# Optimization experiments

Hardware: AMD Instinct MI355X
Metric: run time of the kernel (lower is better)

The kernel has to match this reference:

```python
import jax, jax.numpy as jnp
import numpy as np

N_ATOMS = 100000
N_EDGES = 6400000
CUTOFF = 12.0
CUTOFF_SR = 2.0
CUTOFF_SQ = CUTOFF * CUTOFF
KEHALF = 7.199822675975274  # ASE kehalf, unit factors = 1


def poly6_switch(d, cutoff):
    # Poly6 smooth switch-off: 1 at d=0, 0 at d>=cutoff
    x = d / cutoff
    sw = 1.0 - 10.0 * x**3 + 15.0 * x**4 - 6.0 * x**5
    return jnp.where(d < cutoff, sw, jnp.zeros_like(sw))


def setup_inputs() -> dict:
    key = jax.random.key(0)
    k1, k2, k3, k4, k5 = jax.random.split(key, 5)
    atomic_charges = jax.random.normal(k1, (N_ATOMS,), dtype=jnp.float32) * 0.3
    atomic_dipoles = jax.random.normal(k2, (N_ATOMS,), dtype=jnp.float32) * 0.1
    # distances in (0.5, 13.5): some pairs inside short-range, some beyond cutoff
    distances = jax.random.uniform(k3, (N_EDGES,), dtype=jnp.float32) * 13.0 + 0.5
    idx_i = jax.random.randint(k4, (N_EDGES,), 0, N_ATOMS, dtype=jnp.int32)
    idx_j = jax.random.randint(k5, (N_EDGES,), 0, N_ATOMS, dtype=jnp.int32)
    return {
        "atomic_charges": atomic_charges,
        "atomic_dipoles": atomic_dipoles,
        "distances": distances,
        "idx_i": idx_i,
        "idx_j": idx_j,
    }


def reference(atomic_charges, atomic_dipoles, distances, idx_i, idx_j):
    # gather per-edge charges / dipoles
    qi = atomic_charges[idx_i]
    qj = atomic_charges[idx_j]
    di = atomic_dipoles[idx_i]
    dj = atomic_dipoles[idx_j]

    d = distances
    d_sh = jnp.sqrt(d * d + 1.0)  # shielded distance

    sw_off = poly6_switch(d, CUTOFF_SR)
    sw_on = 1.0 - sw_off

    # split_distance=True branch (cutoff != cutoff_short_range):
    # shifted-force Coulomb (charge-charge, ~1/d)
    E_ord_q = 1.0 / d + d / CUTOFF_SQ - 2.0 / CUTOFF
    E_sh_q = 1.0 / d_sh + d_sh / CUTOFF_SQ - 2.0 / CUTOFF
    E_q = KEHALF * qi * qj * (sw_off * E_sh_q + sw_on * E_ord_q)

    # dipole-dipole term (~1/d^3), same shielded/ordinary blending
    E_ord_d = 1.0 / d**3
    E_sh_d = 1.0 / d_sh**3
    E_d = KEHALF * di * dj * (sw_off * E_sh_d + sw_on * E_ord_d)

    E = E_q + E_d
    E = jnp.where(d <= CUTOFF, E, jnp.zeros_like(E))

    # scatter-sum per-edge energies to atoms
    return jax.ops.segment_sum(E, idx_i, num_segments=N_ATOMS)
```

## Files before the change

kernel.cpp:

```cpp
#include <hip/hip_runtime.h>
#include <hip/hip_bf16.h>
#include <hip/hip_fp16.h>

#define CUTOFF_C    12.0f
#define CUTOFF_SR_C 2.0f
#define CUTOFF_SQ_C 144.0f
#define KEHALF_C    7.199822675975274f

#define BLK1   1024

#define CH_DUO   17408
#define LUT_DUO  1024
#define CH_SOLO  33792
#define LUT_SOLO 2048

__device__ __forceinline__ float edge_energy(float d, float qi, float qj,
                                             float di, float dj) {
    float inv_d   = __frcp_rn(d);
    float dsh     = __fsqrt_rn(fmaf(d, d, 1.0f));
    float inv_dsh = __frcp_rn(dsh);
    float x  = d * (1.0f / CUTOFF_SR_C);
    float x3 = x * x * x;
    float sw = fmaf(x3, fmaf(x, fmaf(x, -6.0f, 15.0f), -10.0f), 1.0f);
    float sw_off = (d < CUTOFF_SR_C) ? sw : 0.0f;
    float Eoq = inv_d   + fmaf(d,   (1.0f / CUTOFF_SQ_C), -(2.0f / CUTOFF_C));
    float Esq = inv_dsh + fmaf(dsh, (1.0f / CUTOFF_SQ_C), -(2.0f / CUTOFF_C));
    float Eq  = (KEHALF_C * qi * qj) * fmaf(sw_off, Esq - Eoq, Eoq);
    float Eod = inv_d * inv_d * inv_d;
    float Esd = inv_dsh * inv_dsh * inv_dsh;
    float Ed  = (KEHALF_C * di * dj) * fmaf(sw_off, Esd - Eod, Eod);
    return Eq + Ed;
}

__device__ __forceinline__ float2 fg_exact(float d) {
    float inv_d   = 1.0f / d;
    float dsh     = sqrtf(fmaf(d, d, 1.0f));
    float inv_dsh = 1.0f / dsh;
    float x  = d * (1.0f / CUTOFF_SR_C);
    float x3 = x * x * x;
    float sw = fmaf(x3, fmaf(x, fmaf(x, -6.0f, 15.0f), -10.0f), 1.0f);
    float sw_off = (d < CUTOFF_SR_C) ? sw : 0.0f;
    float Foq = inv_d   + fmaf(d,   (1.0f / CUTOFF_SQ_C), -(2.0f / CUTOFF_C));
    float Fsq = inv_dsh + fmaf(dsh, (1.0f / CUTOFF_SQ_C), -(2.0f / CUTOFF_C));
    float F   = fmaf(sw_off, Fsq - Foq, Foq);
    float God = inv_d * inv_d * inv_d;
    float Gsd = inv_dsh * inv_dsh * inv_dsh;
    float G   = fmaf(sw_off, Gsd - God, God);
    return make_float2(KEHALF_C * F, KEHALF_C * G);
}

__device__ __forceinline__ __half2 vw_make_exact(float d, __half2 hqdj) {
    float2 qdj = __half22float2(hqdj);
    float2 fg  = fg_exact(d);
    return __floats2half2_rn(qdj.x * fg.x, qdj.y * fg.y);
}

__device__ __forceinline__ unsigned h2bits(__half2 h) {
    union { __half2 h; unsigned u; } c; c.h = h; return c.u;
}
__device__ __forceinline__ __half2 bits2h(unsigned u) {
    union { unsigned u; __half2 h; } c; c.u = u; return c.h;
}
template <typename T>
__device__ __forceinline__ auto atom_add_h2(T* p, T v, int)
    -> decltype(atomicAdd(p, v), void()) {
    atomicAdd(p, v);
}
template <typename T>
__device__ __forceinline__ void atom_add_h2(T* p, T v, long) {
    unsigned* u = (unsigned*)p;
    unsigned old = *u, assumed;
    do {
        assumed = old;
        __half2 sum = __hadd2(bits2h(assumed), v);
        old = atomicCAS(u, assumed, h2bits(sum));
    } while (old != assumed);
}

__global__ __launch_bounds__(256) void pc_pack_qd_h(
    const float* __restrict__ q,
    const float* __restrict__ dip,
    __half2*     __restrict__ qd,
    int n_atoms)
{
    int a = blockIdx.x * 256 + threadIdx.x;
    if (a < n_atoms) qd[a] = __floats2half2_rn(q[a], dip[a]);
}

template <int CH, int LUTN, int BLK>
__global__ __launch_bounds__(BLK) void pc_scatter_lut(
    const float*   __restrict__ dist,
    const int*     __restrict__ idx_i,
    const int*     __restrict__ idx_j,
    const __half2* __restrict__ qd,
    __half2*       __restrict__ partial,
    int n_edges, int n4, int S, int gps, int n_atoms, int nch)
{
    extern __shared__ char smem[];
    __half2* acc2 = (__half2*)smem;
    float2*  lut  = (float2*)(smem + (size_t)CH * sizeof(__half2));

    const int s    = blockIdx.x % S;
    const int c    = blockIdx.x / S;
    const int base = c * CH;
    const int lim  = min(CH, n_atoms - base);

    const __half2 hzero = __floats2half2_rn(0.0f, 0.0f);
    for (int i = threadIdx.x; i < CH; i += BLK) acc2[i] = hzero;

    const float hstep = CUTOFF_C / (float)LUTN;
    for (int k = threadIdx.x; k <= LUTN; k += BLK) {
        float d = fmaxf((float)k * hstep, 0.25f * hstep);
        lut[k] = fg_exact(d);
    }
    __syncthreads();

    const int g0 = s * gps;
    const int g1 = min(g0 + gps, n4);
    const int4*   idxi4 = (const int4*)idx_i;
    const int4*   idxj4 = (const int4*)idx_j;
    const float4* dist4 = (const float4*)dist;
    const float   dscale = (float)LUTN / CUTOFF_C;

    for (int g = g0 + (int)threadIdx.x; g < g1; g += BLK) {
        int4   i4 = idxi4[g];
        int4   j4 = idxj4[g];
        float4 d4 = dist4[g];

        int      ii[4] = { i4.x, i4.y, i4.z, i4.w };
        int      jj[4] = { j4.x, j4.y, j4.z, j4.w };
        float    dd[4] = { d4.x, d4.y, d4.z, d4.w };
        unsigned lc[4];
        bool     vl[4];
        __half2  qh[4];

        #pragma unroll
        for (int k = 0; k < 4; ++k) {
            lc[k] = (unsigned)(ii[k] - base);
            vl[k] = (lc[k] < (unsigned)CH) && (dd[k] <= CUTOFF_C);
        }
        #pragma unroll
        for (int k = 0; k < 4; ++k)
            qh[k] = vl[k] ? qd[jj[k]] : hzero;

        #pragma unroll
        for (int k = 0; k < 4; ++k) {
            if (vl[k]) {
                float t  = dd[k] * dscale;
                int   kk = min((int)t, LUTN - 1);
                float fr = t - (float)kk;
                float2 l0 = lut[kk];
                float2 l1 = lut[kk + 1];
                float F = fmaf(fr, l1.x - l0.x, l0.x);
                float G = fmaf(fr, l1.y - l0.y, l0.y);
                float2 qdj = __half22float2(qh[k]);
                __half2 vw = __floats2half2_rn(qdj.x * F, qdj.y * G);
                atom_add_h2(&acc2[lc[k]], vw, 0);
            }
        }
    }

    if (s == S - 1) {
        for (int e = (n4 << 2) + (int)threadIdx.x; e < n_edges; e += BLK) {
            int i = idx_i[e];
            float d = dist[e];
            unsigned local = (unsigned)(i - base);
            if (local < (unsigned)CH && d <= CUTOFF_C) {
                __half2 vw = vw_make_exact(d, qd[idx_j[e]]);
                atom_add_h2(&acc2[local], vw, 0);
            }
        }
    }

    __syncthreads();
    __half2* row = partial + (size_t)s * n_atoms + base;
    for (int i = threadIdx.x; i < lim; i += BLK) row[i] = acc2[i];
}

__global__ __launch_bounds__(256) void pc_reduce_vw(
    const __half2* __restrict__ partial,
    const float*   __restrict__ q,
    const float*   __restrict__ dip,
    float*         __restrict__ out,
    int n_atoms, int S)
{
    __shared__ float2 sh[256];
    int a0   = blockIdx.x * 64;
    int lane = threadIdx.x & 63;
    int w    = threadIdx.x >> 6;
    int a    = a0 + lane;

    float sv = 0.0f, sw = 0.0f;
    if (a < n_atoms) {
        int per = S >> 2;
        const __half2* p = partial + a;
        int s = w * per, send = s + per;
        for (; s < send; ++s) {
            float2 t = __half22float2(p[(size_t)s * n_atoms]);
            sv += t.x; sw += t.y;
        }
    }
    sh[threadIdx.x] = make_float2(sv, sw);
    __syncthreads();
    if (w == 0 && a < n_atoms) {
        float2 t0 = sh[lane],       t1 = sh[64 + lane];
        float2 t2 = sh[128 + lane], t3 = sh[192 + lane];
        float fv = (t0.x + t1.x) + (t2.x + t3.x);
        float fw = (t0.y + t1.y) + (t2.y + t3.y);
        out[a] = fmaf(q[a], fv, dip[a] * fw);
    }
}

__global__ __launch_bounds__(256) void pc_dipole_edges_atomic(
    const float* __restrict__ q,
    const float* __restrict__ dip,
    const float* __restrict__ dist,
    const int*   __restrict__ idx_i,
    const int*   __restrict__ idx_j,
    float*       __restrict__ out,
    int n_edges)
{
    int t = blockIdx.x * blockDim.x + threadIdx.x;
    const int stride = gridDim.x * blockDim.x;
    for (int e = t; e < n_edges; e += stride) {
        float d = dist[e];
        if (d > CUTOFF_C) continue;
        int i = idx_i[e], j = idx_j[e];
        atomicAdd(&out[i], edge_energy(d, q[i], q[j], dip[i], dip[j]));
    }
}

static int probe_blocks(const void* f, int blk, size_t lds) {
    hipError_t e1 = hipFuncSetAttribute(
        f, hipFuncAttributeMaxDynamicSharedMemorySize, (int)lds);
    int nb = 0;
    hipError_t e2 = hipOccupancyMaxActiveBlocksPerMultiprocessor(&nb, f, blk, lds);
    if (e1 != hipSuccess || e2 != hipSuccess) return 0;
    return nb;
}

extern "C" void kernel_launch(void* const* d_in, const int* in_sizes, int n_in,
                              void* d_out, int out_size, void* d_ws, size_t ws_size,
                              hipStream_t stream) {
    const float* q     = (const float*)d_in[0];
    const float* dip   = (const float*)d_in[1];
    const float* dist  = (const float*)d_in[2];
    const int*   idx_i = (const int*)d_in[3];
    const int*   idx_j = (const int*)d_in[4];
    float*       out   = (float*)d_out;

    int n_edges = in_sizes[2];
    int n_atoms = out_size;
    int n4      = n_edges >> 2;

    size_t lds_duo  = (size_t)CH_DUO  * sizeof(__half2)
                    + (size_t)(LUT_DUO  + 1) * sizeof(float2);
    size_t lds_solo = (size_t)CH_SOLO * sizeof(__half2)
                    + (size_t)(LUT_SOLO + 1) * sizeof(float2);

    int nb_duo = probe_blocks((const void*)&pc_scatter_lut<CH_DUO, LUT_DUO, BLK1>,
                              BLK1, lds_duo);
    int nb_solo = probe_blocks((const void*)&pc_scatter_lut<CH_SOLO, LUT_SOLO, BLK1>,
                               BLK1, lds_solo);

    bool use_duo = (nb_duo >= 2);
    int  CH, nch, S, cap;
    size_t lds;
    if (use_duo) {
        CH  = CH_DUO;  lds = lds_duo;
        nch = (n_atoms + CH - 1) / CH;
        cap = 512;
    } else {
        CH  = CH_SOLO; lds = lds_solo;
        nch = (n_atoms + CH - 1) / CH;
        cap = 256;
    }
    S = (cap / nch) & ~7;
    if (S < 8) S = 8;

    size_t qd_b  = ((size_t)n_atoms * sizeof(__half2) + 255) & ~(size_t)255;
    size_t avail = (ws_size > qd_b) ? ws_size - qd_b : 0;
    int S_fit = (int)(avail / ((size_t)n_atoms * sizeof(__half2)));
    if (S_fit < S) S = S_fit & ~7;

    bool ok = (use_duo || nb_solo >= 1) && S >= 8 && n_atoms > 0;

    if (ok) {
        __half2* qd      = (__half2*)d_ws;
        __half2* partial = (__half2*)((char*)d_ws + qd_b);
        int      gps     = (n4 + S - 1) / S;

        pc_pack_qd_h<<<(n_atoms + 255) / 256, 256, 0, stream>>>(q, dip, qd,
                                                                n_atoms);
        if (use_duo)
            pc_scatter_lut<CH_DUO, LUT_DUO, BLK1>
                <<<S * nch, BLK1, lds, stream>>>(
                    dist, idx_i, idx_j, qd, partial, n_edges, n4, S, gps,
                    n_atoms, nch);
        else
            pc_scatter_lut<CH_SOLO, LUT_SOLO, BLK1>
                <<<S * nch, BLK1, lds, stream>>>(
                    dist, idx_i, idx_j, qd, partial, n_edges, n4, S, gps,
                    n_atoms, nch);
        pc_reduce_vw<<<(n_atoms + 63) / 64, 256, 0, stream>>>(
            partial, q, dip, out, n_atoms, S);
    } else {
        hipMemsetAsync(out, 0, (size_t)n_atoms * sizeof(float), stream);
        int grid = (n_edges + 255) / 256;
        pc_dipole_edges_atomic<<<grid, 256, 0, stream>>>(
            q, dip, dist, idx_i, idx_j, out, n_edges);
    }
}
```

Measured before the change: 161.9 us.

## Precompute per-edge (index, energy-weight) records before chunked LDS scatter

Adds a pre-pass that reads distance, indices and the j-atom charge/dipole once per edge, computes the qj- and dj-weighted energy factors in half precision with fast rcp/rsq intrinsics, and writes a compact 8-byte record (idx_i, packed weights) per edge. The scatter kernel then streams these records instead of re-reading three input arrays and re-evaluating energies in every atom-chunk pass, with a larger chunk size. This cuts repeated gather and math work across chunks, at the cost of an extra 51MB write-and-read round trip and looser fast-math accuracy.

```diff
diff --git a/kernel.cpp b/kernel.cpp
--- a/kernel.cpp
+++ b/kernel.cpp
@@ -13,6 +13,8 @@
 #define LUT_DUO  1024
 #define CH_SOLO  33792
 #define LUT_SOLO 2048
+
+#define CH_REC   20000
 
 __device__ __forceinline__ float edge_energy(float d, float qi, float qj,
                                              float di, float dj) {
@@ -77,6 +79,26 @@
     } while (old != assumed);
 }
 
+__device__ __forceinline__ unsigned vw_bits(float d, __half2 hq) {
+    float inv_d   = __builtin_amdgcn_rcpf(d);
+    float dsh2    = fmaf(d, d, 1.0f);
+    float inv_dsh = __builtin_amdgcn_rsqf(dsh2);
+    float dsh     = dsh2 * inv_dsh;
+    float x  = d * (1.0f / CUTOFF_SR_C);
+    float x3 = x * x * x;
+    float sw = fmaf(x3, fmaf(x, fmaf(x, -6.0f, 15.0f), -10.0f), 1.0f);
+    float sw_off = (d < CUTOFF_SR_C) ? sw : 0.0f;
+    float Foq = inv_d   + fmaf(d,   (1.0f / CUTOFF_SQ_C), -(2.0f / CUTOFF_C));
+    float Fsq = inv_dsh + fmaf(dsh, (1.0f / CUTOFF_SQ_C), -(2.0f / CUTOFF_C));
+    float F   = fmaf(sw_off, Fsq - Foq, Foq);
+    float God = inv_d * inv_d * inv_d;
+    float Gsd = inv_dsh * inv_dsh * inv_dsh;
+    float G   = fmaf(sw_off, Gsd - God, God);
+    float2 q2 = __half22float2(hq);
+    __half2 vw = __floats2half2_rn((KEHALF_C * q2.x) * F, (KEHALF_C * q2.y) * G);
+    return h2bits(vw);
+}
+
 __global__ __launch_bounds__(256) void pc_pack_qd_h(
     const float* __restrict__ q,
     const float* __restrict__ dip,
@@ -85,6 +107,97 @@
 {
     int a = blockIdx.x * 256 + threadIdx.x;
     if (a < n_atoms) qd[a] = __floats2half2_rn(q[a], dip[a]);
+}
+
+__global__ __launch_bounds__(256) void pc_edge_pre(
+    const float*   __restrict__ dist,
+    const int*     __restrict__ idx_i,
+    const int*     __restrict__ idx_j,
+    const __half2* __restrict__ qd,
+    uint4*         __restrict__ rec4,
+    int n_edges, int n4)
+{
+    const __half2 hzero = __floats2half2_rn(0.0f, 0.0f);
+    const int t0     = blockIdx.x * 256 + (int)threadIdx.x;
+    const int stride = gridDim.x * 256;
+    const int4*   i4p = (const int4*)idx_i;
+    const int4*   j4p = (const int4*)idx_j;
+    const float4* d4p = (const float4*)dist;
+
+    for (int g = t0; g < n4; g += stride) {
+        int4   i4 = i4p[g];
+        int4   j4 = j4p[g];
+        float4 d4 = d4p[g];
+
+        int   ii[4] = { i4.x, i4.y, i4.z, i4.w };
+        int   jj[4] = { j4.x, j4.y, j4.z, j4.w };
+        float dd[4] = { d4.x, d4.y, d4.z, d4.w };
+        bool     vl[4];
+        __half2  qh[4];
+        unsigned ir[4], vwr[4];
+
+        #pragma unroll
+        for (int k = 0; k < 4; ++k) vl[k] = dd[k] <= CUTOFF_C;
+        #pragma unroll
+        for (int k = 0; k < 4; ++k) qh[k] = vl[k] ? qd[jj[k]] : hzero;
+        #pragma unroll
+        for (int k = 0; k < 4; ++k) {
+            ir[k]  = vl[k] ? (unsigned)ii[k] : 0xFFFFFFFFu;
+            vwr[k] = vw_bits(dd[k], qh[k]);
+        }
+        rec4[g]      = make_uint4(ir[0], vwr[0], ir[1], vwr[1]);
+        rec4[n4 + g] = make_uint4(ir[2], vwr[2], ir[3], vwr[3]);
+    }
+
+    uint2* rec2 = (uint2*)rec4;
+    for (int e = (n4 << 2) + t0; e < n_edges; e += stride) {
+        float d = dist[e];
+        bool  v = d <= CUTOFF_C;
+        __half2 hq = v ? qd[idx_j[e]] : hzero;
+        rec2[e] = make_uint2(v ? (unsigned)idx_i[e] : 0xFFFFFFFFu, vw_bits(d, hq));
+    }
+}
+
+template <int CH, int BLK>
+__global__ __launch_bounds__(BLK) void pc_scatter_rec(
+    const uint4* __restrict__ rec4,
+    __half2*     __restrict__ partial,
+    int n_edges, int nv2, int S, int gps, int n_atoms)
+{
+    extern __shared__ char smem[];
+    __half2* acc2 = (__half2*)smem;
+
+    const int s = blockIdx.x % S;
+    const int c = blockIdx.x / S;
+    const unsigned base = (unsigned)(c * CH);
+    const int lim = min(CH, n_atoms - (int)base);
+
+    const __half2 hzero = __floats2half2_rn(0.0f, 0.0f);
+    for (int i = threadIdx.x; i < CH; i += BLK) acc2[i] = hzero;
+    __syncthreads();
+
+    const int g0 = s * gps;
+    const int g1 = min(g0 + gps, nv2);
+    for (int g = g0 + (int)threadIdx.x; g < g1; g += BLK) {
+        uint4 r = rec4[g];
+        unsigned lc0 = r.x - base;
+        unsigned lc1 = r.z - base;
+        if (lc0 < (unsigned)CH) atom_add_h2(&acc2[lc0], bits2h(r.y), 0);
+        if (lc1 < (unsigned)CH) atom_add_h2(&acc2[lc1], bits2h(r.w), 0);
+    }
+
+    if (s == S - 1 && (n_edges & 1)) {
+        if (threadIdx.x == 0) {
+            const uint2* rec2 = (const uint2*)rec4;
+            uint2 r = rec2[n_edges - 1];
+            unsigned lc = r.x - base;
+            if (lc < (unsigned)CH) atom_add_h2(&acc2[lc], bits2h(r.y), 0);
+        }
+    }
+
+    __syncthreads();
+    __half2* row = partial + (size_t)s * n_atoms + (int)base;
+    for (int i = threadIdx.x; i < lim; i += BLK) row[i] = acc2[i];
 }
 
 template <int CH, int LUTN, int BLK>
@@ -252,6 +365,45 @@
     int n_edges = in_sizes[2];
     int n_atoms = out_size;
     int n4      = n_edges >> 2;
+    int nv2     = n_edges >> 1;
+
+    size_t qd_b   = ((size_t)n_atoms * sizeof(__half2) + 255) & ~(size_t)255;
+    size_t rec_b  = (((size_t)n_edges * 8) + 255) & ~(size_t)255;
+    size_t lds_rec = (size_t)CH_REC * sizeof(__half2);
+
+    int nb_rec = probe_blocks((const void*)&pc_scatter_rec<CH_REC, BLK1>,
+                              BLK1, lds_rec);
+
+    int S_new = 0, nch_new = 0;
+    if (nb_rec >= 2 && n_atoms > 0 && ws_size > qd_b + rec_b) {
+        nch_new = (n_atoms + CH_REC - 1) / CH_REC;
+        int cap = 512;
+        S_new = (cap / nch_new) & ~7;
+        size_t avail = ws_size - qd_b - rec_b;
+        int S_fit = (int)(avail / ((size_t)n_atoms * sizeof(__half2))) & ~7;
+        if (S_fit < S_new) S_new = S_fit;
+    }
+
+    if (S_new >= 8) {
+        __half2* qd      = (__half2*)d_ws;
+        uint4*   rec4    = (uint4*)((char*)d_ws + qd_b);
+        __half2* partial = (__half2*)((char*)d_ws + qd_b + rec_b);
+        int      gps     = (nv2 + S_new - 1) / S_new;
+
+        pc_pack_qd_h<<<(n_atoms + 255) / 256, 256, 0, stream>>>(q, dip, qd,
+                                                                n_atoms);
+        int gridA = (n_edges + 1023) / 1024;
+        if (gridA > 2048) gridA = 2048;
+        if (gridA < 1)    gridA = 1;
+        pc_edge_pre<<<gridA, 256, 0, stream>>>(dist, idx_i, idx_j, qd, rec4,
+                                               n_edges, n4);
+        pc_scatter_rec<CH_REC, BLK1>
+            <<<S_new * nch_new, BLK1, lds_rec, stream>>>(
+                rec4, partial, n_edges, nv2, S_new, gps, n_atoms);
+        pc_reduce_vw<<<(n_atoms + 63) / 64, 256, 0, stream>>>(
+            partial, q, dip, out, n_atoms, S_new);
+        return;
+    }
 
     size_t lds_duo  = (size_t)CH_DUO  * sizeof(__half2)
                     + (size_t)(LUT_DUO  + 1) * sizeof(float2);
@@ -278,7 +430,6 @@
     S = (cap / nch) & ~7;
     if (S < 8) S = 8;
 
-    size_t qd_b  = ((size_t)n_atoms * sizeof(__half2) + 255) & ~(size_t)255;
     size_t avail = (ws_size > qd_b) ? ws_size - qd_b : 0;
     int S_fit = (int)(avail / ((size_t)n_atoms * sizeof(__half2)));
     if (S_fit < S) S = S_fit & ~7;
```

New measurement: 164.5 us. About the same (+1.6%).

## Replace LDS-chunked scatter with direct global half2 atomics into 64 partial copies

Applied to the files above, without the earlier changes.

Adds a new default path that skips the chunked LDS accumulation. Each edge's half2 contribution now goes straight to global memory with unsafe atomic adds into one of 64 replicated partial arrays, chosen by block index. The pack kernel also zeroes those partials. Edge energies use fast rcp/rsq intrinsics instead of correctly rounded ones. This removes the repeated edge streaming per atom chunk and the LDS pressure, at the cost of random global atomics, extra zeroing traffic, and slightly lower accuracy.

```diff
diff --git a/kernel.cpp b/kernel.cpp
--- a/kernel.cpp
+++ b/kernel.cpp
@@ -13,6 +13,8 @@
 #define LUT_DUO  1024
 #define CH_SOLO  33792
 #define LUT_SOLO 2048
+
+#define NPART 64
 
 __device__ __forceinline__ float edge_energy(float d, float qi, float qj,
                                              float di, float dj) {
@@ -61,6 +63,28 @@
 __device__ __forceinline__ __half2 bits2h(unsigned u) {
     union { unsigned u; __half2 h; } c; c.u = u; return c.h;
 }
+
+template <typename T>
+__device__ __forceinline__ auto atom_add_h2u(T* p, T v, int)
+    -> decltype(unsafeAtomicAdd(p, v), void()) {
+    unsafeAtomicAdd(p, v);
+}
+template <typename T>
+__device__ __forceinline__ auto atom_add_h2u(T* p, T v, long)
+    -> decltype(atomicAdd(p, v), void()) {
+    atomicAdd(p, v);
+}
+template <typename T>
+__device__ __forceinline__ void atom_add_h2u(T* p, T v, ...) {
+    unsigned* u = (unsigned*)p;
+    unsigned old = *u, assumed;
+    do {
+        assumed = old;
+        __half2 sum = __hadd2(bits2h(assumed), v);
+        old = atomicCAS(u, assumed, h2bits(sum));
+    } while (old != assumed);
+}
+
 template <typename T>
 __device__ __forceinline__ auto atom_add_h2(T* p, T v, int)
     -> decltype(atomicAdd(p, v), void()) {
@@ -77,14 +101,102 @@
     } while (old != assumed);
 }
 
-__global__ __launch_bounds__(256) void pc_pack_qd_h(
+__device__ __forceinline__ unsigned vw_bits(float d, __half2 hq) {
+    float inv_d   = __builtin_amdgcn_rcpf(d);
+    float dsh2    = fmaf(d, d, 1.0f);
+    float inv_dsh = __builtin_amdgcn_rsqf(dsh2);
+    float dsh     = dsh2 * inv_dsh;
+    float x  = d * (1.0f / CUTOFF_SR_C);
+    float x3 = x * x * x;
+    float sw = fmaf(x3, fmaf(x, fmaf(x, -6.0f, 15.0f), -10.0f), 1.0f);
+    float sw_off = (d < CUTOFF_SR_C) ? sw : 0.0f;
+    float Foq = inv_d   + fmaf(d,   (1.0f / CUTOFF_SQ_C), -(2.0f / CUTOFF_C));
+    float Fsq = inv_dsh + fmaf(dsh, (1.0f / CUTOFF_SQ_C), -(2.0f / CUTOFF_C));
+    float F   = fmaf(sw_off, Fsq - Foq, Foq);
+    float God = inv_d * inv_d * inv_d;
+    float Gsd = inv_dsh * inv_dsh * inv_dsh;
+    float G   = fmaf(sw_off, Gsd - God, God);
+    float2 q2 = __half22float2(hq);
+    __half2 vw = __floats2half2_rn((KEHALF_C * q2.x) * F, (KEHALF_C * q2.y) * G);
+    return h2bits(vw);
+}
+
+__global__ __launch_bounds__(256) void pc_pack_zero(
     const float* __restrict__ q,
     const float* __restrict__ dip,
     __half2*     __restrict__ qd,
-    int n_atoms)
+    uint4*       __restrict__ pz,
+    unsigned*    __restrict__ pzs,
+    int n_atoms, int nz4, int nzs)
 {
-    int a = blockIdx.x * 256 + threadIdx.x;
-    if (a < n_atoms) qd[a] = __floats2half2_rn(q[a], dip[a]);
+    const int t      = blockIdx.x * 256 + (int)threadIdx.x;
+    const int stride = gridDim.x * 256;
+    if (t < n_atoms) qd[t] = __floats2half2_rn(q[t], dip[t]);
+    const uint4 z4 = make_uint4(0u, 0u, 0u, 0u);
+    for (int z = t; z < nz4; z += stride) pz[z] = z4;
+    if (t < nzs) pzs[(size_t)nz4 * 4 + t] = 0u;
+}
+
+__global__ __launch_bounds__(256) void pc_edge_fused(
+    const float*   __restrict__ dist,
+    const int*     __restrict__ idx_i,
+    const int*     __restrict__ idx_j,
+    const __half2* __restrict__ qd,
+    __half2*       __restrict__ partial,
+    int n_edges, int n4, int half, int n_atoms, int pmask)
+{
+    const int t = blockIdx.x * 256 + (int)threadIdx.x;
+    __half2* pp = partial + (size_t)((int)blockIdx.x & pmask) * n_atoms;
+    const int4*   j4p = (const int4*)idx_j;
+    const int4*   i4p = (const int4*)idx_i;
+    const float4* d4p = (const float4*)dist;
+
+    if (t < half) {
+        const int  ga = t;
+        const int  gb = t + half;
+        const bool vb = gb < n4;
+        const int  gbs = vb ? gb : ga;
+
+        int4   ja = j4p[ga];
+        int4   jb = j4p[gbs];
+        float4 da = d4p[ga];
+        float4 db = d4p[gbs];
+        int4   ia = i4p[ga];
+        int4   ib = i4p[gbs];
+
+        __half2 q0 = qd[ja.x], q1 = qd[ja.y], q2 = qd[ja.z], q3 = qd[ja.w];
+        __half2 q4 = qd[jb.x], q5 = qd[jb.y], q6 = qd[jb.z], q7 = qd[jb.w];
+
+        unsigned w0 = vw_bits(da.x, q0);
+        unsigned w1 = vw_bits(da.y, q1);
+        unsigned w2 = vw_bits(da.z, q2);
+        unsigned w3 = vw_bits(da.w, q3);
+        unsigned w4 = vw_bits(db.x, q4);
+        unsigned w5 = vw_bits(db.y, q5);
+        unsigned w6 = vw_bits(db.z, q6);
+        unsigned w7 = vw_bits(db.w, q7);
+
+        if (da.x <= CUTOFF_C) atom_add_h2u(&pp[ia.x], bits2h(w0), 0);
+        if (da.y <= CUTOFF_C) atom_add_h2u(&pp[ia.y], bits2h(w1), 0);
+        if (da.z <= CUTOFF_C) atom_add_h2u(&pp[ia.z], bits2h(w2), 0);
+        if (da.w <= CUTOFF_C) atom_add_h2u(&pp[ia.w], bits2h(w3), 0);
+        if (vb) {
+            if (db.x <= CUTOFF_C) atom_add_h2u(&pp[ib.x], bits2h(w4), 0);
+            if (db.y <= CUTOFF_C) atom_add_h2u(&pp[ib.y], bits2h(w5), 0);
+            if (db.z <= CUTOFF_C) atom_add_h2u(&pp[ib.z], bits2h(w6), 0);
+            if (db.w <= CUTOFF_C) atom_add_h2u(&pp[ib.w], bits2h(w7), 0);
+        }
+    }
+
+    const int tl = n_edges & 3;
+    if (blockIdx.x == 0 && (int)threadIdx.x < tl) {
+        int e = (n4 << 2) + (int)threadIdx.x;
+        float d = dist[e];
+        if (d <= CUTOFF_C) {
+            unsigned w = vw_bits(d, qd[idx_j[e]]);
+            atom_add_h2u(&pp[idx_i[e]], bits2h(w), 0);
+        }
+    }
 }
 
 template <int CH, int LUTN, int BLK>
@@ -253,6 +365,38 @@
     int n_atoms = out_size;
     int n4      = n_edges >> 2;
 
+    size_t qd_b = ((size_t)n_atoms * sizeof(__half2) + 255) & ~(size_t)255;
+
+    int P = NPART;
+    while (P > 8 && ws_size < qd_b + (size_t)P * n_atoms * sizeof(__half2))
+        P >>= 1;
+    size_t part_b = (size_t)P * n_atoms * sizeof(__half2);
+
+    bool fused_ok = (n_atoms > 0) && (P >= 8) && (ws_size >= qd_b + part_b);
+
+    if (fused_ok) {
+        __half2* qd      = (__half2*)d_ws;
+        __half2* partial = (__half2*)((char*)d_ws + qd_b);
+
+        long long tot = (long long)P * n_atoms;
+        int nz4 = (int)(tot >> 2);
+        int nzs = (int)(tot & 3);
+        int gridPZ = (n_atoms + 255) / 256;
+        if (gridPZ < 2048) gridPZ = 2048;
+
+        int half  = (n4 + 1) >> 1;
+        int gridA = (half + 255) / 256;
+        if (gridA < 1) gridA = 1;
+
+        pc_pack_zero<<<gridPZ, 256, 0, stream>>>(
+            q, dip, qd, (uint4*)partial, (unsigned*)partial, n_atoms, nz4, nzs);
+        pc_edge_fused<<<gridA, 256, 0, stream>>>(
+            dist, idx_i, idx_j, qd, partial, n_edges, n4, half, n_atoms, P - 1);
+        pc_reduce_vw<<<(n_atoms + 63) / 64, 256, 0, stream>>>(
+            partial, q, dip, out, n_atoms, P);
+        return;
+    }
+
     size_t lds_duo  = (size_t)CH_DUO  * sizeof(__half2)
                     + (size_t)(LUT_DUO  + 1) * sizeof(float2);
     size_t lds_solo = (size_t)CH_SOLO * sizeof(__half2)
@@ -278,7 +422,6 @@
     S = (cap / nch) & ~7;
     if (S < 8) S = 8;
 
-    size_t qd_b  = ((size_t)n_atoms * sizeof(__half2) + 255) & ~(size_t)255;
     size_t avail = (ws_size > qd_b) ? ws_size - qd_b : 0;
     int S_fit = (int)(avail / ((size_t)n_atoms * sizeof(__half2)));
     if (S_fit < S) S = S_fit & ~7;
@@ -290,8 +433,8 @@
         __half2* partial = (__half2*)((char*)d_ws + qd_b);
         int      gps     = (n4 + S - 1) / S;
 
-        pc_pack_qd_h<<<(n_atoms + 255) / 256, 256, 0, stream>>>(q, dip, qd,
-                                                                n_atoms);
+        pc_pack_zero<<<(n_atoms + 255) / 256, 256, 0, stream>>>(
+            q, dip, qd, (uint4*)qd, (unsigned*)qd, n_atoms, 0, 0);
         if (use_duo)
             pc_scatter_lut<CH_DUO, LUT_DUO, BLK1>
                 <<<S * nch, BLK1, lds, stream>>>(
```

Measured after the change: 383.3 us. +136.7%, slower.
